# Kernel tuning notes

Hardware: AMD Instinct MI355X
Metric: run time of the kernel (lower is better)

Reference implementation:

```python
import jax, jax.numpy as jnp
import numpy as np

EMB = 1024
HEAD = 128

def setup_inputs() -> dict:
    key = jax.random.key(0)
    kx, kk, kq, kv = jax.random.split(key, 4)
    s = 1.0 / np.sqrt(EMB)
    return {
        "x": jax.random.normal(kx, (8, 2048, EMB), dtype=jnp.float32),
        "Wk": jax.random.normal(kk, (EMB, HEAD), dtype=jnp.float32) * s,
        "Wq": jax.random.normal(kq, (EMB, HEAD), dtype=jnp.float32) * s,
        "Wv": jax.random.normal(kv, (EMB, HEAD), dtype=jnp.float32) * s,
    }

def reference(x, Wk, Wq, Wv):
    # x: [B,T,E]; projections (no bias)
    k = jnp.einsum('bte,eh->bth', x, Wk)
    q = jnp.einsum('bte,eh->bth', x, Wq)
    v = jnp.einsum('bte,eh->bth', x, Wv)
    # scores: [B,T,T], NOTE: no 1/sqrt(d) scaling in original module
    qk = jnp.einsum('bih,bjh->bij', q, k)
    T = x.shape[1]
    causal = jnp.tril(jnp.ones((T, T), dtype=bool))  # True = keep
    qk = jnp.where(causal, qk, -jnp.inf)
    # NOTE: softmax over axis -2 (query axis), as in original
    attn = jax.nn.softmax(qk, axis=-2)
    return jnp.einsum('bij,bjh->bih', attn, v)
```

## Files before the change

kernel.cpp:

```cpp
#include <hip/hip_runtime.h>

typedef unsigned short u16;
typedef unsigned int u32;
typedef _Float16 f16;
typedef __attribute__((ext_vector_type(8))) _Float16 f16x8;
typedef __attribute__((ext_vector_type(4))) float f32x4;

constexpr int SEQ = 2048;
constexpr int EMBD = 1024;
constexpr int HD = 128;
constexpr int NB = 8;
constexpr int NSL = 8;

__device__ inline u16 f2h(float f) { return __builtin_bit_cast(u16, (f16)f); }
__device__ inline u32 pack2(float a, float b) { return (u32)f2h(a) | ((u32)f2h(b) << 16); }

__device__ inline f32x4 mfma16(f16x8 a, f16x8 b, f32x4 c) {
  return __builtin_amdgcn_mfma_f32_16x16x32_f16(a, b, c, 0, 0, 0);
}

__device__ __forceinline__ void gload16(const u16* g, u16* l) {
  __builtin_amdgcn_global_load_lds(
      (const __attribute__((address_space(1))) u32*)g,
      (__attribute__((address_space(3))) u32*)l, 16, 0, 0);
}

template<int RB>
__device__ inline f16x8 frag_ld(const u16* lds, int row, int e) {
  int byte = row * RB + ((e * 2) ^ ((row & 7) << 4));
  return *reinterpret_cast<const f16x8*>(reinterpret_cast<const char*>(lds) + byte);
}

__global__ __launch_bounds__(256) void k_cvt_w(const float* __restrict__ Wq,
                                               const float* __restrict__ Wk,
                                               const float* __restrict__ Wv,
                                               u16* __restrict__ Wt) {
  int t = blockIdx.x * 256 + threadIdx.x;
  int e0 = (t & 255) * 4;
  int H = t >> 8;
  int w = H >> 7, h = H & 127;
  const float* W = (w == 0) ? Wq : (w == 1) ? Wk : Wv;
  ushort4 o;
  o.x = f2h(W[(size_t)(e0 + 0) * HD + h]);
  o.y = f2h(W[(size_t)(e0 + 1) * HD + h]);
  o.z = f2h(W[(size_t)(e0 + 2) * HD + h]);
  o.w = f2h(W[(size_t)(e0 + 3) * HD + h]);
  int k0t = e0 >> 6, ec = e0 & 63;
  size_t el = (size_t)(k0t * 384 + H) * 64 + (ec ^ ((H & 7) << 3));
  *reinterpret_cast<ushort4*>(Wt + el) = o;
}

__global__ __launch_bounds__(512, 4) void k_proj(const float* __restrict__ x,
                                                 const u16* __restrict__ Wt,
                                                 u16* __restrict__ Qb,
                                                 u16* __restrict__ Kb,
                                                 u16* __restrict__ Vtb) {
  __shared__ __align__(16) u16 As[2][64 * 64];
  __shared__ __align__(16) u16 Bs[2][192 * 64];
  const int mt = blockIdx.x, ny = blockIdx.y;
  const int t = threadIdx.x, lane = t & 63, wave = t >> 6;
  const int rh = (wave & 1) * 32, cq = (wave >> 1) * 48;
  const int ar = t >> 3, ac = t & 7;
  const float* asrc = x + (size_t)(mt * 64 + ar) * EMBD + ac * 8;
  const int adst = ar * 64 + ((ac * 8) ^ ((ar & 7) << 3));
  f32x4 zero = {0.f, 0.f, 0.f, 0.f};
  f32x4 acc[2][3];
#pragma unroll
  for (int a = 0; a < 2; ++a)
#pragma unroll
    for (int b = 0; b < 3; ++b) acc[a][b] = zero;

  {
#pragma unroll
    for (int q = 0; q < 3; ++q) {
      int lin = q * 512 + t;
      gload16(Wt + ny * 12288 + lin * 8, &Bs[0][lin * 8]);
    }
    float4 a0 = *reinterpret_cast<const float4*>(asrc);
    float4 a1 = *reinterpret_cast<const float4*>(asrc + 4);
    uint4 o = {pack2(a0.x, a0.y), pack2(a0.z, a0.w), pack2(a1.x, a1.y), pack2(a1.z, a1.w)};
    *reinterpret_cast<uint4*>(&As[0][adst]) = o;
  }
  __syncthreads();
  int cur = 0;
  for (int s = 0; s < 16; ++s) {
    float4 a0, a1;
    const bool pf = (s < 15);
    if (pf) {
#pragma unroll
      for (int q = 0; q < 3; ++q) {
        int lin = q * 512 + t;
        gload16(Wt + (s + 1) * 24576 + ny * 12288 + lin * 8, &Bs[cur ^ 1][lin * 8]);
      }
      a0 = *reinterpret_cast<const float4*>(asrc + (s + 1) * 64);
      a1 = *reinterpret_cast<const float4*>(asrc + (s + 1) * 64 + 4);
    }
#pragma unroll
    for (int kk = 0; kk < 2; ++kk) {
      f16x8 af0 = frag_ld<128>(As[cur], rh + (lane & 15), kk * 32 + (lane >> 4) * 8);
      f16x8 af1 = frag_ld<128>(As[cur], rh + 16 + (lane & 15), kk * 32 + (lane >> 4) * 8);
#pragma unroll
      for (int fc = 0; fc < 3; ++fc) {
        f16x8 bw = frag_ld<128>(Bs[cur], cq + fc * 16 + (lane & 15), kk * 32 + (lane >> 4) * 8);
        acc[0][fc] = mfma16(af0, bw, acc[0][fc]);
        acc[1][fc] = mfma16(af1, bw, acc[1][fc]);
      }
    }
    if (pf) {
      uint4 o = {pack2(a0.x, a0.y), pack2(a0.z, a0.w), pack2(a1.x, a1.y), pack2(a1.z, a1.w)};
      *reinterpret_cast<uint4*>(&As[cur ^ 1][adst]) = o;
    }
    __syncthreads();
    cur ^= 1;
  }
#pragma unroll
  for (int fi = 0; fi < 2; ++fi)
#pragma unroll
    for (int fc = 0; fc < 3; ++fc) {
      int gcol = ny * 192 + cq + fc * 16 + (lane & 15);
      int w = gcol >> 7, h = gcol & 127;
      int i0 = mt * 64 + rh + fi * 16 + (lane >> 4) * 4;
      if (w < 2) {
        u16* P = w ? Kb : Qb;
#pragma unroll
        for (int r = 0; r < 4; ++r) {
          int i = i0 + r;
          P[(size_t)i * 128 + (h ^ ((i & 7) << 3))] = f2h(acc[fi][fc][r]);
        }
      } else {
        int bb = i0 >> 11, jt = (i0 >> 6) & 31, tl = i0 & 63;
        ushort4 o = {f2h(acc[fi][fc][0]), f2h(acc[fi][fc][1]),
                     f2h(acc[fi][fc][2]), f2h(acc[fi][fc][3])};
        size_t el = ((size_t)(bb * 32 + jt) * 128 + h) * 64 + (tl ^ ((h & 7) << 3));
        *reinterpret_cast<ushort4*>(Vtb + el) = o;
      }
    }
}

__device__ inline void merge_ml(float& m, float& l, float m2, float l2) {
  float mn = fmaxf(m, m2);
  float a = (m > -1e37f) ? l * __expf(m - mn) : 0.f;
  float b = (m2 > -1e37f) ? l2 * __expf(m2 - mn) : 0.f;
  m = mn;
  l = a + b;
}

__global__ __launch_bounds__(256, 2) void k_statsA(const u16* __restrict__ Qb,
                                                   const u16* __restrict__ Kb,
                                                   float* __restrict__ mpart,
                                                   float* __restrict__ lpart) {
  __shared__ __align__(16) u16 Qs[2][128 * 128];
  const int id = blockIdx.y * 64 + blockIdx.x;
  const int bb = id & 7, z = (id >> 3) & 7, sl = id >> 6;
  const int t = threadIdx.x, lane = t & 63, wj = (t >> 6) * 32;
  f32x4 zero = {0.f, 0.f, 0.f, 0.f};

  for (int ph = 0; ph < 2; ++ph) {
    const int jt = ph ? 15 - z : z;
    __syncthreads();
#pragma unroll
    for (int q = 0; q < 8; ++q) {
      int lin = q * 256 + t;
      gload16(Kb + ((size_t)bb * SEQ + jt * 128) * 128 + lin * 8, &Qs[0][lin * 8]);
    }
    __syncthreads();
    f16x8 af[2][4];
#pragma unroll
    for (int fj = 0; fj < 2; ++fj)
#pragma unroll
      for (int kk = 0; kk < 4; ++kk)
        af[fj][kk] = frag_ld<256>(Qs[0], wj + fj * 16 + (lane & 15), kk * 32 + (lane >> 4) * 8);
    float m[2][4], l[2][4];
#pragma unroll
    for (int a = 0; a < 2; ++a)
#pragma unroll
      for (int r = 0; r < 4; ++r) {
        m[a][r] = -INFINITY;
        l[a][r] = 0.f;
      }
    const int it0 = jt + ((sl - jt) & 7);
    int cur = 1;
    if (it0 < 16) {
#pragma unroll
      for (int q = 0; q < 8; ++q) {
        int lin = q * 256 + t;
        gload16(Qb + ((size_t)bb * SEQ + it0 * 128) * 128 + lin * 8, &Qs[1][lin * 8]);
      }
      for (int it = it0; it < 16; it += 8) {
        __syncthreads();
        if (it + 8 < 16) {
#pragma unroll
          for (int q = 0; q < 8; ++q) {
            int lin = q * 256 + t;
            gload16(Qb + ((size_t)bb * SEQ + (it + 8) * 128) * 128 + lin * 8,
                    &Qs[cur ^ 1][lin * 8]);
          }
        }
        f32x4 acc[2][8];
#pragma unroll
        for (int a = 0; a < 2; ++a)
#pragma unroll
          for (int b = 0; b < 8; ++b) acc[a][b] = zero;
#pragma unroll
        for (int kk = 0; kk < 4; ++kk)
#pragma unroll
          for (int fi = 0; fi < 8; ++fi) {
            f16x8 bq = frag_ld<256>(Qs[cur], fi * 16 + (lane & 15), kk * 32 + (lane >> 4) * 8);
            acc[0][fi] = mfma16(af[0][kk], bq, acc[0][fi]);
            acc[1][fi] = mfma16(af[1][kk], bq, acc[1][fi]);
          }
#pragma unroll
        for (int fj = 0; fj < 2; ++fj)
#pragma unroll
          for (int r = 0; r < 4; ++r) {
            int jg = jt * 128 + wj + fj * 16 + (lane >> 4) * 4 + r;
            float v[8];
            float vmax = -INFINITY;
#pragma unroll
            for (int fi = 0; fi < 8; ++fi) {
              int ig = it * 128 + fi * 16 + (lane & 15);
              v[fi] = (ig >= jg) ? acc[fj][fi][r] : -INFINITY;
              vmax = fmaxf(vmax, v[fi]);
            }
            if (vmax > -1e37f) {
              float mn = fmaxf(m[fj][r], vmax);
              float sc = (m[fj][r] > -1e37f) ? __expf(m[fj][r] - mn) : 0.f;
              float ss = 0.f;
#pragma unroll
              for (int fi = 0; fi < 8; ++fi)
                ss += (v[fi] > -1e37f) ? __expf(v[fi] - mn) : 0.f;
              l[fj][r] = l[fj][r] * sc + ss;
              m[fj][r] = mn;
            }
          }
        cur ^= 1;
      }
    }
#pragma unroll
    for (int fj = 0; fj < 2; ++fj)
#pragma unroll
      for (int r = 0; r < 4; ++r)
        for (int msk = 1; msk <= 8; msk <<= 1) {
          float m2 = __shfl_xor(m[fj][r], msk);
          float l2 = __shfl_xor(l[fj][r], msk);
          merge_ml(m[fj][r], l[fj][r], m2, l2);
        }
    if ((lane & 15) == 0) {
#pragma unroll
      for (int fj = 0; fj < 2; ++fj)
#pragma unroll
        for (int r = 0; r < 4; ++r) {
          int j = jt * 128 + wj + fj * 16 + (lane >> 4) * 4 + r;
          size_t idx = (size_t)sl * (NB * SEQ) + (size_t)bb * SEQ + j;
          mpart[idx] = m[fj][r];
          lpart[idx] = l[fj][r];
        }
    }
  }
}

__global__ __launch_bounds__(256) void k_stats_reduce(const float* __restrict__ mpart,
                                                      const float* __restrict__ lpart,
                                                      float* __restrict__ Mg,
                                                      float* __restrict__ RLg) {
  int idx = blockIdx.x * 256 + threadIdx.x;
  float m = -INFINITY;
#pragma unroll
  for (int sl = 0; sl < NSL; sl++) m = fmaxf(m, mpart[sl * (NB * SEQ) + idx]);
  float l = 0.f;
#pragma unroll
  for (int sl = 0; sl < NSL; sl++) {
    float ms = mpart[sl * (NB * SEQ) + idx];
    if (ms > -1e37f) l += lpart[sl * (NB * SEQ) + idx] * __expf(ms - m);
  }
  Mg[idx] = m;
  RLg[idx] = 1.0f / l;
}

__global__ __launch_bounds__(256, 2) void k_passB(const u16* __restrict__ Qb,
                                                  const u16* __restrict__ Kb,
                                                  const u16* __restrict__ Vtb,
                                                  const float* __restrict__ Mg,
                                                  const float* __restrict__ RLg,
                                                  u16* __restrict__ opart) {
  __shared__ __align__(16) u16 Ks2[2][64 * 128];
  __shared__ __align__(16) u16 Vs2[2][128 * 64];
  const int id = blockIdx.y * 64 + blockIdx.x;
  const int bb = id & 7, z = (id >> 3) & 7, sl = id >> 6;
  const int t = threadIdx.x, lane = t & 63, wi = (t >> 6) * 32;
  f32x4 zero = {0.f, 0.f, 0.f, 0.f};

  auto stageKV = [&](int jt, int b) {
#pragma unroll
    for (int q = 0; q < 4; ++q) {
      int lin = q * 256 + t;
      gload16(Kb + ((size_t)bb * SEQ + jt * 64) * 128 + lin * 8, &Ks2[b][lin * 8]);
    }
#pragma unroll
    for (int q = 0; q < 4; ++q) {
      int lin = q * 256 + t;
      gload16(Vtb + ((size_t)bb * 32 + jt) * 8192 + lin * 8, &Vs2[b][lin * 8]);
    }
  };

  for (int ph = 0; ph < 2; ++ph) {
    const int it = ph ? 15 - z : z;
    f16x8 qf[2][4];
#pragma unroll
    for (int fi = 0; fi < 2; ++fi)
#pragma unroll
      for (int kk = 0; kk < 4; ++kk) {
        size_t gi = (size_t)bb * SEQ + it * 128 + wi + fi * 16 + (lane & 15);
        int e0 = kk * 32 + (lane >> 4) * 8;
        qf[fi][kk] = *reinterpret_cast<const f16x8*>(Qb + gi * 128 + (e0 ^ (((int)gi & 7) << 3)));
      }
    f32x4 accO[2][8];
#pragma unroll
    for (int a = 0; a < 2; ++a)
#pragma unroll
      for (int b = 0; b < 8; ++b) accO[a][b] = zero;
    const int jtmax = 2 * it + 1;
    int cur = 0;
    __syncthreads();
    if (sl <= jtmax) stageKV(sl, 0);
    for (int jt = sl; jt <= jtmax; jt += 8) {
      __syncthreads();
      float mjv[4], rlv[4];
#pragma unroll
      for (int fj = 0; fj < 4; ++fj) {
        int jg = jt * 64 + fj * 16 + (lane & 15);
        mjv[fj] = Mg[bb * SEQ + jg];
        rlv[fj] = RLg[bb * SEQ + jg];
      }
      f32x4 accS[2][4];
#pragma unroll
      for (int a = 0; a < 2; ++a)
#pragma unroll
        for (int b = 0; b < 4; ++b) accS[a][b] = zero;
#pragma unroll
      for (int kk = 0; kk < 4; ++kk)
#pragma unroll
        for (int fj = 0; fj < 4; ++fj) {
          f16x8 bk = frag_ld<256>(Ks2[cur], fj * 16 + (lane & 15), kk * 32 + (lane >> 4) * 8);
          accS[0][fj] = mfma16(qf[0][kk], bk, accS[0][fj]);
          accS[1][fj] = mfma16(qf[1][kk], bk, accS[1][fj]);
        }
      __syncthreads();
      if (jt + 8 <= jtmax) stageKV(jt + 8, cur ^ 1);
      u16* Ps = Ks2[cur];
#pragma unroll
      for (int fj = 0; fj < 4; ++fj) {
        int jloc = fj * 16 + (lane & 15);
        int jg = jt * 64 + jloc;
        float mj = mjv[fj], rlj = rlv[fj];
#pragma unroll
        for (int fi = 0; fi < 2; ++fi)
#pragma unroll
          for (int r = 0; r < 4; ++r) {
            int iloc = wi + fi * 16 + (lane >> 4) * 4 + r;
            int ig = it * 128 + iloc;
            float p = __expf(accS[fi][fj][r] - mj) * rlj;
            if (ig < jg) p = 0.f;
            Ps[iloc * 64 + (jloc ^ ((iloc & 7) << 3))] = f2h(p);
          }
      }
#pragma unroll
      for (int ks = 0; ks < 2; ++ks) {
        f16x8 pa0 = frag_ld<128>(Ps, wi + (lane & 15), ks * 32 + (lane >> 4) * 8);
        f16x8 pa1 = frag_ld<128>(Ps, wi + 16 + (lane & 15), ks * 32 + (lane >> 4) * 8);
#pragma unroll
        for (int fh = 0; fh < 8; ++fh) {
          f16x8 bv = frag_ld<128>(Vs2[cur], fh * 16 + (lane & 15), ks * 32 + (lane >> 4) * 8);
          accO[0][fh] = mfma16(pa0, bv, accO[0][fh]);
          accO[1][fh] = mfma16(pa1, bv, accO[1][fh]);
        }
      }
      cur ^= 1;
    }
#pragma unroll
    for (int fi = 0; fi < 2; ++fi)
#pragma unroll
      for (int fh = 0; fh < 8; ++fh)
#pragma unroll
        for (int r = 0; r < 4; ++r) {
          int ig = it * 128 + wi + fi * 16 + (lane >> 4) * 4 + r;
          int h = fh * 16 + (lane & 15);
          opart[(((size_t)sl * NB + bb) * SEQ + ig) * HD + h] = f2h(accO[fi][fh][r]);
        }
  }
}

__global__ __launch_bounds__(256) void k_reduceB(const u16* __restrict__ opart,
                                                 float* __restrict__ out) {
  size_t base = ((size_t)blockIdx.x * 256 + threadIdx.x) * 8;
  const size_t S = (size_t)NB * SEQ * HD;
  float s[8];
#pragma unroll
  for (int j = 0; j < 8; j++) s[j] = 0.f;
#pragma unroll
  for (int sl = 0; sl < NSL; sl++) {
    f16x8 v = *reinterpret_cast<const f16x8*>(opart + sl * S + base);
#pragma unroll
    for (int j = 0; j < 8; j++) s[j] += (float)v[j];
  }
  float4 o0 = {s[0], s[1], s[2], s[3]};
  float4 o1 = {s[4], s[5], s[6], s[7]};
  *reinterpret_cast<float4*>(out + base) = o0;
  *reinterpret_cast<float4*>(out + base + 4) = o1;
}

extern "C" void kernel_launch(void* const* d_in, const int* in_sizes, int n_in,
                              void* d_out, int out_size, void* d_ws, size_t ws_size,
                              hipStream_t stream) {
  (void)in_sizes; (void)n_in; (void)out_size; (void)ws_size;
  const float* x = (const float*)d_in[0];
  const float* Wk = (const float*)d_in[1];
  const float* Wq = (const float*)d_in[2];
  const float* Wv = (const float*)d_in[3];
  float* out = (float*)d_out;
  char* ws = (char*)d_ws;

  u16* Wt = (u16*)(ws + 0);
  u16* Qb = (u16*)(ws + 786432);
  u16* Kb = (u16*)(ws + 4980736);
  u16* Vtb = (u16*)(ws + 9175040);
  float* mpart = (float*)(ws + 13369344);
  float* lpart = (float*)(ws + 13893632);
  float* Mg = (float*)(ws + 14417920);
  float* RLg = (float*)(ws + 14483456);
  u16* opart = (u16*)(ws + 14548992);

  k_cvt_w<<<384, 256, 0, stream>>>(Wq, Wk, Wv, Wt);
  k_proj<<<dim3(256, 2), 512, 0, stream>>>(x, Wt, Qb, Kb, Vtb);
  k_statsA<<<dim3(64, 8), 256, 0, stream>>>(Qb, Kb, mpart, lpart);
  k_stats_reduce<<<64, 256, 0, stream>>>(mpart, lpart, Mg, RLg);
  k_passB<<<dim3(64, 8), 256, 0, stream>>>(Qb, Kb, Vtb, Mg, RLg, opart);
  k_reduceB<<<1024, 256, 0, stream>>>(opart, out);
}
```

Before: 84.67 us.

## Give P its own LDS buffer, prefetch KV earlier, fold softmax stats

In passB, P now goes into its own LDS buffer instead of reusing the current K buffer. That removes the mid-iteration barrier and lets the next K/V tile prefetch start right after the loop-top barrier, so it overlaps the QK^T MFMAs. The max and reciprocal-sum statistics are folded into one per-column constant m+log(l), which removes one global load and one multiply per element. s_setprio raises wave priority around the MFMA loops in both statsA and passB. The extra buffer adds 16KB of LDS per block, which could limit occupancy, and computing exp(s - c) changes rounding slightly.

Result: no change. 83.82 us (-1.0%).

```diff
diff --git a/kernel.cpp b/kernel.cpp
--- a/kernel.cpp
+++ b/kernel.cpp
@@ -201,6 +201,7 @@
         for (int a = 0; a < 2; ++a)
 #pragma unroll
           for (int b = 0; b < 8; ++b) acc[a][b] = zero;
+        __builtin_amdgcn_s_setprio(1);
 #pragma unroll
         for (int kk = 0; kk < 4; ++kk)
 #pragma unroll
@@ -209,6 +210,7 @@
             acc[0][fi] = mfma16(af[0][kk], bq, acc[0][fi]);
             acc[1][fi] = mfma16(af[1][kk], bq, acc[1][fi]);
           }
+        __builtin_amdgcn_s_setprio(0);
 #pragma unroll
         for (int fj = 0; fj < 2; ++fj)
 #pragma unroll
@@ -261,8 +263,7 @@
 
 __global__ __launch_bounds__(256) void k_stats_reduce(const float* __restrict__ mpart,
                                                       const float* __restrict__ lpart,
-                                                      float* __restrict__ Mg,
-                                                      float* __restrict__ RLg) {
+                                                      float* __restrict__ Cg) {
   int idx = blockIdx.x * 256 + threadIdx.x;
   float m = -INFINITY;
 #pragma unroll
@@ -273,18 +274,17 @@
     float ms = mpart[sl * (NB * SEQ) + idx];
     if (ms > -1e37f) l += lpart[sl * (NB * SEQ) + idx] * __expf(ms - m);
   }
-  Mg[idx] = m;
-  RLg[idx] = 1.0f / l;
+  Cg[idx] = m + __logf(l);
 }
 
 __global__ __launch_bounds__(256, 2) void k_passB(const u16* __restrict__ Qb,
                                                   const u16* __restrict__ Kb,
                                                   const u16* __restrict__ Vtb,
-                                                  const float* __restrict__ Mg,
-                                                  const float* __restrict__ RLg,
+                                                  const float* __restrict__ Cg,
                                                   u16* __restrict__ opart) {
   __shared__ __align__(16) u16 Ks2[2][64 * 128];
   __shared__ __align__(16) u16 Vs2[2][128 * 64];
+  __shared__ __align__(16) u16 Ps[128 * 64];
   const int id = blockIdx.y * 64 + blockIdx.x;
   const int bb = id & 7, z = (id >> 3) & 7, sl = id >> 6;
   const int t = threadIdx.x, lane = t & 63, wi = (t >> 6) * 32;
@@ -320,23 +320,22 @@
 #pragma unroll
       for (int b = 0; b < 8; ++b) accO[a][b] = zero;
     const int jtmax = 2 * it + 1;
-    int cur = 0;
     __syncthreads();
     if (sl <= jtmax) stageKV(sl, 0);
+    int cur = 0;
     for (int jt = sl; jt <= jtmax; jt += 8) {
       __syncthreads();
-      float mjv[4], rlv[4];
-#pragma unroll
-      for (int fj = 0; fj < 4; ++fj) {
-        int jg = jt * 64 + fj * 16 + (lane & 15);
-        mjv[fj] = Mg[bb * SEQ + jg];
-        rlv[fj] = RLg[bb * SEQ + jg];
-      }
+      if (jt + 8 <= jtmax) stageKV(jt + 8, cur ^ 1);
+      float cj[4];
+#pragma unroll
+      for (int fj = 0; fj < 4; ++fj)
+        cj[fj] = Cg[bb * SEQ + jt * 64 + fj * 16 + (lane & 15)];
       f32x4 accS[2][4];
 #pragma unroll
       for (int a = 0; a < 2; ++a)
 #pragma unroll
         for (int b = 0; b < 4; ++b) accS[a][b] = zero;
+      __builtin_amdgcn_s_setprio(1);
 #pragma unroll
       for (int kk = 0; kk < 4; ++kk)
 #pragma unroll
@@ -345,25 +344,24 @@
           accS[0][fj] = mfma16(qf[0][kk], bk, accS[0][fj]);
           accS[1][fj] = mfma16(qf[1][kk], bk, accS[1][fj]);
         }
-      __syncthreads();
-      if (jt + 8 <= jtmax) stageKV(jt + 8, cur ^ 1);
-      u16* Ps = Ks2[cur];
+      __builtin_amdgcn_s_setprio(0);
 #pragma unroll
       for (int fj = 0; fj < 4; ++fj) {
         int jloc = fj * 16 + (lane & 15);
         int jg = jt * 64 + jloc;
-        float mj = mjv[fj], rlj = rlv[fj];
+        float c = cj[fj];
 #pragma unroll
         for (int fi = 0; fi < 2; ++fi)
 #pragma unroll
           for (int r = 0; r < 4; ++r) {
             int iloc = wi + fi * 16 + (lane >> 4) * 4 + r;
             int ig = it * 128 + iloc;
-            float p = __expf(accS[fi][fj][r] - mj) * rlj;
+            float p = __expf(accS[fi][fj][r] - c);
             if (ig < jg) p = 0.f;
             Ps[iloc * 64 + (jloc ^ ((iloc & 7) << 3))] = f2h(p);
           }
       }
+      __builtin_amdgcn_s_setprio(1);
 #pragma unroll
       for (int ks = 0; ks < 2; ++ks) {
         f16x8 pa0 = frag_ld<128>(Ps, wi + (lane & 15), ks * 32 + (lane >> 4) * 8);
@@ -375,6 +373,7 @@
           accO[1][fh] = mfma16(pa1, bv, accO[1][fh]);
         }
       }
+      __builtin_amdgcn_s_setprio(0);
       cur ^= 1;
     }
 #pragma unroll
@@ -426,14 +425,13 @@
   u16* Vtb = (u16*)(ws + 9175040);
   float* mpart = (float*)(ws + 13369344);
   float* lpart = (float*)(ws + 13893632);
-  float* Mg = (float*)(ws + 14417920);
-  float* RLg = (float*)(ws + 14483456);
+  float* Cg = (float*)(ws + 14417920);
   u16* opart = (u16*)(ws + 14548992);
 
   k_cvt_w<<<384, 256, 0, stream>>>(Wq, Wk, Wv, Wt);
   k_proj<<<dim3(256, 2), 512, 0, stream>>>(x, Wt, Qb, Kb, Vtb);
   k_statsA<<<dim3(64, 8), 256, 0, stream>>>(Qb, Kb, mpart, lpart);
-  k_stats_reduce<<<64, 256, 0, stream>>>(mpart, lpart, Mg, RLg);
-  k_passB<<<dim3(64, 8), 256, 0, stream>>>(Qb, Kb, Vtb, Mg, RLg, opart);
+  k_stats_reduce<<<64, 256, 0, stream>>>(mpart, lpart, Cg);
+  k_passB<<<dim3(64, 8), 256, 0, stream>>>(Qb, Kb, Vtb, Cg, opart);
   k_reduceB<<<1024, 256, 0, stream>>>(opart, out);
 }
```
